# Performance work log

Hardware: AMD Instinct MI355X
Metric: run time of the kernel (lower is better)

Reference implementation:

```python
import jax, jax.numpy as jnp
import numpy as np

H = 512   # n_hidden
V = 32000 # n_words
T1 = 128  # encoder length
T2 = 64   # decoder length
B = 32    # batch


def _gru_cell(x, h, W_ih, W_hh, b_ih, b_hh):
    # PyTorch GRUCell math. x: [B, in], h: [B, H]
    gi = x @ W_ih.T + b_ih            # [B, 3H]
    gh = h @ W_hh.T + b_hh            # [B, 3H]
    i_r, i_z, i_n = jnp.split(gi, 3, axis=-1)
    h_r, h_z, h_n = jnp.split(gh, 3, axis=-1)
    r = jax.nn.sigmoid(i_r + h_r)
    z = jax.nn.sigmoid(i_z + h_z)
    n = jnp.tanh(i_n + r * h_n)
    return (1.0 - z) * n + z * h


def setup_inputs() -> dict:
    key = jax.random.key(0)
    ks = jax.random.split(key, 18)
    s = 0.05
    f32 = jnp.float32
    return {
        "decoder_inputs": jax.random.randint(ks[0], (T2, B), 0, V),
        "state": jax.random.normal(ks[1], (2, B, H), f32),
        "encoder_outputs": jax.random.normal(ks[2], (T1, B, H), f32),
        "emb": jax.random.normal(ks[3], (V, H), f32) * s,
        "wa_W": jax.random.normal(ks[4], (H, 2 * H), f32) * s,
        "wa_b": jax.random.normal(ks[5], (H,), f32) * s,
        "va_W": jax.random.normal(ks[6], (1, H), f32) * s,
        "W_ih0": jax.random.normal(ks[7], (3 * H, 2 * H), f32) * s,
        "W_hh0": jax.random.normal(ks[8], (3 * H, H), f32) * s,
        "b_ih0": jax.random.normal(ks[9], (3 * H,), f32) * s,
        "b_hh0": jax.random.normal(ks[10], (3 * H,), f32) * s,
        "W_ih1": jax.random.normal(ks[11], (3 * H, H), f32) * s,
        "W_hh1": jax.random.normal(ks[12], (3 * H, H), f32) * s,
        "b_ih1": jax.random.normal(ks[13], (3 * H,), f32) * s,
        "b_hh1": jax.random.normal(ks[14], (3 * H,), f32) * s,
        "out_W": jax.random.normal(ks[15], (V, H), f32) * s,
        "out_b": jax.random.normal(ks[16], (V,), f32) * s,
    }


def reference(decoder_inputs, state, encoder_outputs, emb, wa_W, wa_b, va_W,
              W_ih0, W_hh0, b_ih0, b_hh0, W_ih1, W_hh1, b_ih1, b_hh1,
              out_W, out_b):
    x = emb[decoder_inputs]                               # [T2, B, H]
    # wa(concat([xt_rep, enc])) == xt @ Wx.T + enc @ We.T + b  (split the weight)
    Wx = wa_W[:, :H]                                      # [H, H]
    We = wa_W[:, H:]                                      # [H, H]
    enc_proj = jnp.einsum('tbh,oh->tbo', encoder_outputs, We) + wa_b  # [T1,B,H]
    va = va_W[0]                                          # [H]

    def step(h, xt):  # h: [2,B,H], xt: [B,H]
        u = jnp.tanh(xt @ Wx.T + enc_proj)                # [T1, B, H]
        e = jnp.einsum('tbh,h->tb', u, va)                # [T1, B]
        score = jax.nn.softmax(e, axis=0)                 # softmax over T1
        att_v = jnp.einsum('tbh,tb->bh', encoder_outputs, score)  # [B, H]
        gin = jnp.concatenate([xt, att_v], axis=-1)       # [B, 2H]
        h0 = _gru_cell(gin, h[0], W_ih0, W_hh0, b_ih0, b_hh0)
        h1 = _gru_cell(h0, h[1], W_ih1, W_hh1, b_ih1, b_hh1)
        return jnp.stack([h0, h1]), (h1, score)

    h_final, (ys, scores) = jax.lax.scan(step, state, x)  # ys: [T2, B, H]
    y = jnp.einsum('tbh,vh->tbv', ys, out_W) + out_b      # [T2, B, V]
    last_score = scores[-1][:, :, None]                   # [T1, B, 1] (torch returns last-step score)
    return y, h_final, last_score
```

## Files before the change

### kernel.cpp

```cpp
#include <hip/hip_runtime.h>
#include <hip/hip_bf16.h>
#include <stdint.h>

#define HH   512
#define VV   32000
#define T1N  128
#define T2N  64
#define BB   32

typedef __attribute__((ext_vector_type(8))) short short8;
typedef __attribute__((ext_vector_type(4))) float f32x4;

__device__ __forceinline__ ushort f2b(float f) {
  unsigned u = __float_as_uint(f);
  unsigned r = (u + 0x7fffu + ((u >> 16) & 1u)) >> 16;
  return (ushort)r;
}
__device__ __forceinline__ float blo(unsigned u){ return __uint_as_float(u << 16); }
__device__ __forceinline__ float bhi(unsigned u){ return __uint_as_float(u & 0xffff0000u); }

__device__ __forceinline__ float fast_tanh(float x) {
  float ax = fabsf(x);
  float e  = __expf(-2.f * ax);
  float t  = (1.f - e) / (1.f + e);
  return x < 0.f ? -t : t;
}
__device__ __forceinline__ float fsig(float x) { return 1.f / (1.f + __expf(-x)); }

__global__ __launch_bounds__(256) void k_cvt(const float* __restrict__ s, ushort* __restrict__ d, int n) {
  int i = (blockIdx.x * 256 + threadIdx.x) * 4;
  if (i < n) {
    float4 v = *(const float4*)(s + i);
    ushort4 o = { f2b(v.x), f2b(v.y), f2b(v.z), f2b(v.w) };
    *(ushort4*)(d + i) = o;
  }
}

__global__ __launch_bounds__(256) void k_cvt_wa(const float* __restrict__ wa,
                                                ushort* __restrict__ Wx, ushort* __restrict__ We) {
  int i = (blockIdx.x * 256 + threadIdx.x) * 4;
  int half = (i >= HH * HH);
  int j = i & (HH * HH - 1);
  int o = j >> 9, c = j & 511;
  const float* s = wa + (size_t)o * 1024 + c + (half ? 512 : 0);
  float4 v = *(const float4*)s;
  ushort4 ov = { f2b(v.x), f2b(v.y), f2b(v.z), f2b(v.w) };
  *(ushort4*)((half ? We : Wx) + j) = ov;
}

__global__ __launch_bounds__(256) void k_embed(const int* __restrict__ toks, const float* __restrict__ emb,
                                               ushort* __restrict__ ginB) {
  int i = (blockIdx.x * 256 + threadIdx.x) * 4;
  int row = i >> 9, c = i & 511;
  int tok = toks[row];
  float4 v = *(const float4*)(emb + (size_t)tok * HH + c);
  ushort4 ov = { f2b(v.x), f2b(v.y), f2b(v.z), f2b(v.w) };
  *(ushort4*)(ginB + (size_t)row * 1024 + c) = ov;
}

__global__ __launch_bounds__(256) void k_gemm(const ushort* __restrict__ A, int lda,
                                              const ushort* __restrict__ B,
                                              const float* __restrict__ bias,
                                              float* __restrict__ C, int ldc, int K) {
  __shared__ ushort sA[128 * 32];
  __shared__ ushort sB[128 * 32];
  const int tid  = threadIdx.x;
  const int bm   = blockIdx.y * 128;
  const int bn   = blockIdx.x * 128;
  const int lane = tid & 63;
  const int wave = tid >> 6;
  const int wm   = (wave >> 1) * 64;
  const int wn   = (wave & 1) * 64;
  const int m16  = lane & 15;
  const int quad = lane >> 4;

  f32x4 acc[4][4] = {};

  for (int k0 = 0; k0 < K; k0 += 32) {
#pragma unroll
    for (int q = 0; q < 2; ++q) {
      int idx = q * 256 + tid;
      int row = idx >> 2;
      int kc  = (idx & 3) << 3;
      uint4 va = *(const uint4*)(A + (size_t)(bm + row) * lda + k0 + kc);
      *(uint4*)(&sA[idx * 8]) = va;
      uint4 vb = *(const uint4*)(B + (size_t)(bn + row) * K + k0 + kc);
      *(uint4*)(&sB[idx * 8]) = vb;
    }
    __syncthreads();
    short8 a[4], b[4];
#pragma unroll
    for (int i = 0; i < 4; ++i)
      a[i] = *(const short8*)(&sA[(wm + i * 16 + m16) * 32 + quad * 8]);
#pragma unroll
    for (int j = 0; j < 4; ++j)
      b[j] = *(const short8*)(&sB[(wn + j * 16 + m16) * 32 + quad * 8]);
#pragma unroll
    for (int i = 0; i < 4; ++i)
#pragma unroll
      for (int j = 0; j < 4; ++j)
        acc[i][j] = __builtin_amdgcn_mfma_f32_16x16x32_bf16(a[i], b[j], acc[i][j], 0, 0, 0);
    __syncthreads();
  }
#pragma unroll
  for (int i = 0; i < 4; ++i) {
    int gm = bm + wm + i * 16 + quad * 4;
#pragma unroll
    for (int j = 0; j < 4; ++j) {
      int gn = bn + wn + j * 16 + m16;
      float bv = bias ? bias[gn] : 0.f;
#pragma unroll
      for (int r = 0; r < 4; ++r)
        C[(size_t)(gm + r) * ldc + gn] = acc[i][j][r] + bv;
    }
  }
}

__global__ __launch_bounds__(256) void k_gemm_b16(const ushort* __restrict__ A, int lda,
                                                  const ushort* __restrict__ B,
                                                  const float* __restrict__ bias,
                                                  ushort* __restrict__ C, int ldc, int K) {
  __shared__ ushort sA[128 * 32];
  __shared__ ushort sB[128 * 32];
  const int tid  = threadIdx.x;
  const int bm   = blockIdx.y * 128;
  const int bn   = blockIdx.x * 128;
  const int lane = tid & 63;
  const int wave = tid >> 6;
  const int wm   = (wave >> 1) * 64;
  const int wn   = (wave & 1) * 64;
  const int m16  = lane & 15;
  const int quad = lane >> 4;

  f32x4 acc[4][4] = {};

  for (int k0 = 0; k0 < K; k0 += 32) {
#pragma unroll
    for (int q = 0; q < 2; ++q) {
      int idx = q * 256 + tid;
      int row = idx >> 2;
      int kc  = (idx & 3) << 3;
      uint4 va = *(const uint4*)(A + (size_t)(bm + row) * lda + k0 + kc);
      *(uint4*)(&sA[idx * 8]) = va;
      uint4 vb = *(const uint4*)(B + (size_t)(bn + row) * K + k0 + kc);
      *(uint4*)(&sB[idx * 8]) = vb;
    }
    __syncthreads();
    short8 a[4], b[4];
#pragma unroll
    for (int i = 0; i < 4; ++i)
      a[i] = *(const short8*)(&sA[(wm + i * 16 + m16) * 32 + quad * 8]);
#pragma unroll
    for (int j = 0; j < 4; ++j)
      b[j] = *(const short8*)(&sB[(wn + j * 16 + m16) * 32 + quad * 8]);
#pragma unroll
    for (int i = 0; i < 4; ++i)
#pragma unroll
      for (int j = 0; j < 4; ++j)
        acc[i][j] = __builtin_amdgcn_mfma_f32_16x16x32_bf16(a[i], b[j], acc[i][j], 0, 0, 0);
    __syncthreads();
  }
#pragma unroll
  for (int i = 0; i < 4; ++i) {
    int gm = bm + wm + i * 16 + quad * 4;
#pragma unroll
    for (int j = 0; j < 4; ++j) {
      int gn = bn + wn + j * 16 + m16;
      float bv = bias ? bias[gn] : 0.f;
#pragma unroll
      for (int r = 0; r < 4; ++r)
        C[(size_t)(gm + r) * ldc + gn] = f2b(acc[i][j][r] + bv);
    }
  }
}

__global__ __launch_bounds__(256) void k_scores(const float* __restrict__ xproj,
                                                const float* __restrict__ encp,
                                                const float* __restrict__ vaW,
                                                float* __restrict__ e) {
  int t2g = blockIdx.x >> 5;
  int b   = blockIdx.x & 31;
  __shared__ float sx[4][512];
  int tid = threadIdx.x;
  for (int i = tid; i < 4 * 512; i += 256) {
    int tt = i >> 9, h = i & 511;
    sx[tt][h] = xproj[((size_t)(t2g * 4 + tt) * BB + b) * HH + h];
  }
  __syncthreads();
  int lane = tid & 63, w = tid >> 6;
  int h8 = lane * 8;
  float va[8];
#pragma unroll
  for (int j = 0; j < 8; ++j) va[j] = vaW[h8 + j];
  for (int t1 = w; t1 < T1N; t1 += 4) {
    const float* ep = encp + ((size_t)t1 * BB + b) * HH + h8;
    float ev[8];
    *(float4*)&ev[0] = *(const float4*)ep;
    *(float4*)&ev[4] = *(const float4*)(ep + 4);
    float s0 = 0, s1 = 0, s2 = 0, s3 = 0;
#pragma unroll
    for (int j = 0; j < 8; ++j) {
      float epj = ev[j], vj = va[j];
      s0 += fast_tanh(sx[0][h8 + j] + epj) * vj;
      s1 += fast_tanh(sx[1][h8 + j] + epj) * vj;
      s2 += fast_tanh(sx[2][h8 + j] + epj) * vj;
      s3 += fast_tanh(sx[3][h8 + j] + epj) * vj;
    }
#pragma unroll
    for (int off = 32; off; off >>= 1) {
      s0 += __shfl_down(s0, off);
      s1 += __shfl_down(s1, off);
      s2 += __shfl_down(s2, off);
      s3 += __shfl_down(s3, off);
    }
    if (lane == 0) {
      size_t base = ((size_t)(t2g * 4) * BB + b) * T1N + t1;
      e[base]                 = s0;
      e[base + 1 * BB * T1N]  = s1;
      e[base + 2 * BB * T1N]  = s2;
      e[base + 3 * BB * T1N]  = s3;
    }
  }
}

__global__ __launch_bounds__(128) void k_softmax(const float* __restrict__ e, float* __restrict__ score,
                                                 float* __restrict__ out_last) {
  int row = blockIdx.x;
  int tid = threadIdx.x;
  float v = e[(size_t)row * T1N + tid];
  __shared__ float red[128];
  red[tid] = v; __syncthreads();
  for (int s = 64; s; s >>= 1) { if (tid < s) red[tid] = fmaxf(red[tid], red[tid + s]); __syncthreads(); }
  float mx = red[0]; __syncthreads();
  float p = __expf(v - mx);
  red[tid] = p; __syncthreads();
  for (int s = 64; s; s >>= 1) { if (tid < s) red[tid] += red[tid + s]; __syncthreads(); }
  float sc = p / red[0];
  score[(size_t)row * T1N + tid] = sc;
  if ((row >> 5) == T2N - 1) out_last[tid * BB + (row & 31)] = sc;
}

__global__ __launch_bounds__(256) void k_attv(const float* __restrict__ enc, const float* __restrict__ score,
                                              ushort* __restrict__ ginB) {
  int t2g = blockIdx.x >> 5;
  int b   = blockIdx.x & 31;
  __shared__ float ssc[8][T1N];
  int tid = threadIdx.x;
  for (int i = tid; i < 8 * T1N; i += 256) {
    int j = i >> 7, t1 = i & 127;
    ssc[j][t1] = score[((size_t)(t2g * 8 + j) * BB + b) * T1N + t1];
  }
  __syncthreads();
  float a0[8] = {}, a1[8] = {};
  for (int t1 = 0; t1 < T1N; ++t1) {
    const float* er = enc + ((size_t)t1 * BB + b) * HH;
    float e0 = er[tid], e1 = er[tid + 256];
#pragma unroll
    for (int j = 0; j < 8; ++j) { a0[j] += e0 * ssc[j][t1]; a1[j] += e1 * ssc[j][t1]; }
  }
#pragma unroll
  for (int j = 0; j < 8; ++j) {
    size_t r = (size_t)(t2g * 8 + j) * BB + b;
    ginB[r * 1024 + 512 + tid]       = f2b(a0[j]);
    ginB[r * 1024 + 512 + tid + 256] = f2b(a1[j]);
  }
}

__device__ __forceinline__ void gru_pair(uint gr, uint gz, uint gn, uint hr, uint hz, uint hn,
                                         float hold0, float hold1, float& o0, float& o1) {
  float r0 = fsig(blo(gr) + blo(hr));
  float r1 = fsig(bhi(gr) + bhi(hr));
  float z0 = fsig(blo(gz) + blo(hz));
  float z1 = fsig(bhi(gz) + bhi(hz));
  float n0 = fast_tanh(blo(gn) + r0 * blo(hn));
  float n1 = fast_tanh(bhi(gn) + r1 * bhi(hn));
  o0 = (1.f - z0) * n0 + z0 * hold0;
  o1 = (1.f - z1) * n1 + z1 * hold1;
}

__global__ __launch_bounds__(256) void k_stepA(
    int t,
    const ushort* __restrict__ Whh0B, const ushort* __restrict__ Whh1B,
    const float* __restrict__ bhh0, const float* __restrict__ bhh1,
    const ushort* __restrict__ gi1x, const ushort* __restrict__ gh1x_in,
    const float* __restrict__ h1_in,
    const float* __restrict__ state1,
    const ushort* __restrict__ h0B_in,
    ushort* __restrict__ gh0x_out, ushort* __restrict__ gh1x_out,
    float* __restrict__ h1_out, ushort* __restrict__ ys_out) {
  __shared__ ushort sH1[32 * 520];
  const int tid = threadIdx.x;
  const int blk = blockIdx.x;

  if (t == 0) {
    for (int i = tid; i < 16384; i += 256) {
      int b = i >> 9, k = i & 511;
      sH1[b * 520 + k] = f2b(state1[i]);
    }
  } else {
    const int k0 = tid * 2;
#pragma unroll 4
    for (int b = 0; b < 32; ++b) {
      const ushort* gi = gi1x + b * 1536 + k0;
      const ushort* gh = gh1x_in + b * 1536 + k0;
      uint gir = *(const uint*)(gi);
      uint giz = *(const uint*)(gi + 512);
      uint gin = *(const uint*)(gi + 1024);
      uint hr  = *(const uint*)(gh);
      uint hz  = *(const uint*)(gh + 512);
      uint hn  = *(const uint*)(gh + 1024);
      float2 hold = *(const float2*)(h1_in + b * 512 + k0);
      float o0, o1;
      gru_pair(gir, giz, gin, hr, hz, hn, hold.x, hold.y, o0, o1);
      uint hb = (uint)f2b(o0) | ((uint)f2b(o1) << 16);
      *(uint*)(&sH1[b * 520 + k0]) = hb;
      if (blk == b) {
        *(float2*)(h1_out + b * 512 + k0) = make_float2(o0, o1);
        *(uint*)(ys_out + b * 512 + k0) = hb;
      }
    }
  }
  __syncthreads();

  const int lane = tid & 63, wave = tid >> 6;
  const int bt = wave & 1, nt = wave >> 1;
  const int m16 = lane & 15, quad = lane >> 4;
  const int nrow = blk * 32 + nt * 16 + m16;

  f32x4 acc0 = {0.f, 0.f, 0.f, 0.f}, acc1 = {0.f, 0.f, 0.f, 0.f};
  const ushort* Arow0 = h0B_in + (bt * 16 + m16) * 512 + quad * 8;
  const ushort* Brow0 = Whh0B + (size_t)nrow * 512 + quad * 8;
  const ushort* Brow1 = Whh1B + (size_t)nrow * 512 + quad * 8;
  const ushort* sArow1 = &sH1[(bt * 16 + m16) * 520 + quad * 8];
#pragma unroll 4
  for (int kc = 0; kc < 16; ++kc) {
    short8 a0 = *(const short8*)(Arow0 + kc * 32);
    short8 b0 = *(const short8*)(Brow0 + kc * 32);
    acc0 = __builtin_amdgcn_mfma_f32_16x16x32_bf16(a0, b0, acc0, 0, 0, 0);
    short8 a1 = *(const short8*)(sArow1 + kc * 32);
    short8 b1 = *(const short8*)(Brow1 + kc * 32);
    acc1 = __builtin_amdgcn_mfma_f32_16x16x32_bf16(a1, b1, acc1, 0, 0, 0);
  }
  float bv0 = bhh0[nrow], bv1 = bhh1[nrow];
  int brow = bt * 16 + quad * 4;
#pragma unroll
  for (int r = 0; r < 4; ++r) {
    gh0x_out[(brow + r) * 1536 + nrow] = f2b(acc0[r] + bv0);
    gh1x_out[(brow + r) * 1536 + nrow] = f2b(acc1[r] + bv1);
  }
}

__global__ __launch_bounds__(256) void k_stepB(
    int t,
    const ushort* __restrict__ Wih1B, const float* __restrict__ bih1,
    const ushort* __restrict__ gi0B, const ushort* __restrict__ gh0x,
    const float* __restrict__ h0_in,
    float* __restrict__ h0_out, ushort* __restrict__ h0B_out,
    ushort* __restrict__ gi1x_out) {
  __shared__ ushort sH0[32 * 520];
  const int tid = threadIdx.x;
  const int blk = blockIdx.x;
  const ushort* gi0t = gi0B + (size_t)t * 32 * 1536;

  const int k0 = tid * 2;
#pragma unroll 4
  for (int b = 0; b < 32; ++b) {
    const ushort* gi = gi0t + b * 1536 + k0;
    const ushort* gh = gh0x + b * 1536 + k0;
    uint gir = *(const uint*)(gi);
    uint giz = *(const uint*)(gi + 512);
    uint gin = *(const uint*)(gi + 1024);
    uint hr  = *(const uint*)(gh);
    uint hz  = *(const uint*)(gh + 512);
    uint hn  = *(const uint*)(gh + 1024);
    float2 hold = *(const float2*)(h0_in + b * 512 + k0);
    float o0, o1;
    gru_pair(gir, giz, gin, hr, hz, hn, hold.x, hold.y, o0, o1);
    uint hb = (uint)f2b(o0) | ((uint)f2b(o1) << 16);
    *(uint*)(&sH0[b * 520 + k0]) = hb;
    if (blk == b) {
      *(float2*)(h0_out + b * 512 + k0) = make_float2(o0, o1);
      *(uint*)(h0B_out + b * 512 + k0) = hb;
    }
  }
  __syncthreads();

  const int lane = tid & 63, wave = tid >> 6;
  const int bt = wave & 1, nt = wave >> 1;
  const int m16 = lane & 15, quad = lane >> 4;
  const int nrow = blk * 32 + nt * 16 + m16;

  f32x4 acc = {0.f, 0.f, 0.f, 0.f};
  const ushort* Brow = Wih1B + (size_t)nrow * 512 + quad * 8;
  const ushort* sArow = &sH0[(bt * 16 + m16) * 520 + quad * 8];
#pragma unroll 4
  for (int kc = 0; kc < 16; ++kc) {
    short8 a = *(const short8*)(sArow + kc * 32);
    short8 b = *(const short8*)(Brow + kc * 32);
    acc = __builtin_amdgcn_mfma_f32_16x16x32_bf16(a, b, acc, 0, 0, 0);
  }
  float bv = bih1[nrow];
  int brow = bt * 16 + quad * 4;
#pragma unroll
  for (int r = 0; r < 4; ++r)
    gi1x_out[(brow + r) * 1536 + nrow] = f2b(acc[r] + bv);
}

__global__ __launch_bounds__(256) void k_final(
    const ushort* __restrict__ gi1x, const ushort* __restrict__ gh1x,
    const float* __restrict__ h1_in, const float* __restrict__ h0_fin,
    float* __restrict__ out_h, ushort* __restrict__ ys_out) {
  const int b = blockIdx.x;
  const int k0 = threadIdx.x * 2;
  const ushort* gi = gi1x + b * 1536 + k0;
  const ushort* gh = gh1x + b * 1536 + k0;
  uint gir = *(const uint*)(gi);
  uint giz = *(const uint*)(gi + 512);
  uint gin = *(const uint*)(gi + 1024);
  uint hr  = *(const uint*)(gh);
  uint hz  = *(const uint*)(gh + 512);
  uint hn  = *(const uint*)(gh + 1024);
  float2 hold = *(const float2*)(h1_in + b * 512 + k0);
  float o0, o1;
  gru_pair(gir, giz, gin, hr, hz, hn, hold.x, hold.y, o0, o1);
  *(uint*)(ys_out + b * 512 + k0) = (uint)f2b(o0) | ((uint)f2b(o1) << 16);
  out_h[16384 + b * 512 + k0]     = o0;
  out_h[16384 + b * 512 + k0 + 1] = o1;
  float2 h0p = *(const float2*)(h0_fin + b * 512 + k0);
  *(float2*)(out_h + b * 512 + k0) = h0p;
}

extern "C" void kernel_launch(void* const* d_in, const int* in_sizes, int n_in,
                              void* d_out, int out_size, void* d_ws, size_t ws_size,
                              hipStream_t stream) {
  const int*   toks  = (const int*)d_in[0];
  const float* state = (const float*)d_in[1];
  const float* enc   = (const float*)d_in[2];
  const float* emb   = (const float*)d_in[3];
  const float* wa_W  = (const float*)d_in[4];
  const float* wa_b  = (const float*)d_in[5];
  const float* va    = (const float*)d_in[6];
  const float* b_ih0 = (const float*)d_in[9];
  const float* b_hh0 = (const float*)d_in[10];
  const float* b_ih1 = (const float*)d_in[13];
  const float* b_hh1 = (const float*)d_in[14];
  const float* out_W = (const float*)d_in[15];
  const float* out_b = (const float*)d_in[16];
  const float* W_ih0 = (const float*)d_in[7];
  const float* W_hh0 = (const float*)d_in[8];
  const float* W_ih1 = (const float*)d_in[11];
  const float* W_hh1 = (const float*)d_in[12];

  float* y_out  = (float*)d_out;
  float* h_out  = y_out + (size_t)T2N * BB * VV;
  float* ls_out = h_out + 2 * BB * HH;

  char* ws = (char*)d_ws;
  size_t off = 0;
  auto alloc = [&](size_t bytes) -> void* {
    void* p = ws + off;
    off += (bytes + 255) & ~(size_t)255;
    return p;
  };
  ushort* encB   = (ushort*)alloc((size_t)T1N * BB * HH * 2);
  ushort* ginB   = (ushort*)alloc((size_t)T2N * BB * 2 * HH * 2);
  ushort* WeB    = (ushort*)alloc((size_t)HH * HH * 2);
  ushort* WxB    = (ushort*)alloc((size_t)HH * HH * 2);
  ushort* Wih0B  = (ushort*)alloc((size_t)3 * HH * 2 * HH * 2);
  ushort* Whh0B  = (ushort*)alloc((size_t)3 * HH * HH * 2);
  ushort* Wih1B  = (ushort*)alloc((size_t)3 * HH * HH * 2);
  ushort* Whh1B  = (ushort*)alloc((size_t)3 * HH * HH * 2);
  ushort* outWB  = (ushort*)alloc((size_t)VV * HH * 2);
  ushort* stateB = (ushort*)alloc((size_t)BB * HH * 2);
  float* encproj = (float*)alloc((size_t)T1N * BB * HH * 4);
  float* xproj   = (float*)alloc((size_t)T2N * BB * HH * 4);
  float* eM      = (float*)alloc((size_t)T2N * BB * T1N * 4);
  float* score   = (float*)alloc((size_t)T2N * BB * T1N * 4);
  ushort* gi0B   = (ushort*)alloc((size_t)T2N * BB * 3 * HH * 2);
  ushort* gh0x   = (ushort*)alloc((size_t)BB * 3 * HH * 2);
  ushort* gh1buf0 = (ushort*)alloc((size_t)BB * 3 * HH * 2);
  ushort* gh1buf1 = (ushort*)alloc((size_t)BB * 3 * HH * 2);
  ushort* gi1x   = (ushort*)alloc((size_t)BB * 3 * HH * 2);
  float* h0buf0  = (float*)alloc((size_t)BB * HH * 4);
  float* h0buf1  = (float*)alloc((size_t)BB * HH * 4);
  float* h1buf0  = (float*)alloc((size_t)BB * HH * 4);
  float* h1buf1  = (float*)alloc((size_t)BB * HH * 4);
  ushort* h0bufB0 = (ushort*)alloc((size_t)BB * HH * 2);
  ushort* h0bufB1 = (ushort*)alloc((size_t)BB * HH * 2);
  ushort* ysB    = (ushort*)alloc((size_t)T2N * BB * HH * 2);

  ushort* gh1buf[2]  = {gh1buf0, gh1buf1};
  float*  h0buf[2]   = {h0buf0, h0buf1};
  float*  h1buf[2]   = {h1buf0, h1buf1};
  ushort* h0bufB[2]  = {h0bufB0, h0bufB1};

  k_cvt<<<VV * HH / 1024, 256, 0, stream>>>(out_W, outWB, VV * HH);
  k_cvt<<<T1N * BB * HH / 1024, 256, 0, stream>>>(enc, encB, T1N * BB * HH);
  k_cvt<<<3 * HH * 2 * HH / 1024, 256, 0, stream>>>(W_ih0, Wih0B, 3 * HH * 2 * HH);
  k_cvt<<<3 * HH * HH / 1024, 256, 0, stream>>>(W_hh0, Whh0B, 3 * HH * HH);
  k_cvt<<<3 * HH * HH / 1024, 256, 0, stream>>>(W_ih1, Wih1B, 3 * HH * HH);
  k_cvt<<<3 * HH * HH / 1024, 256, 0, stream>>>(W_hh1, Whh1B, 3 * HH * HH);
  k_cvt<<<BB * HH / 1024, 256, 0, stream>>>(state, stateB, BB * HH);
  k_cvt_wa<<<2 * HH * HH / 1024, 256, 0, stream>>>(wa_W, WxB, WeB);
  k_embed<<<T2N * BB * HH / 1024, 256, 0, stream>>>(toks, emb, ginB);

  k_gemm<<<dim3(HH / 128, T1N * BB / 128), 256, 0, stream>>>(encB, HH, WeB, wa_b, encproj, HH, HH);
  k_gemm<<<dim3(HH / 128, T2N * BB / 128), 256, 0, stream>>>(ginB, 2 * HH, WxB, nullptr, xproj, HH, HH);

  k_scores<<<512, 256, 0, stream>>>(xproj, encproj, va, eM);
  k_softmax<<<T2N * BB, 128, 0, stream>>>(eM, score, ls_out);
  k_attv<<<256, 256, 0, stream>>>(enc, score, ginB);

  k_gemm_b16<<<dim3(3 * HH / 128, T2N * BB / 128), 256, 0, stream>>>(ginB, 2 * HH, Wih0B, b_ih0, gi0B, 3 * HH, 2 * HH);

  for (int t = 0; t < T2N; ++t) {
    const float*  h1_in  = (t <= 1) ? (state + BB * HH) : h1buf[t & 1];
    const ushort* h0B_in = (t == 0) ? stateB : h0bufB[(t + 1) & 1];
    ushort* ys_prev = (t == 0) ? ysB : (ysB + (size_t)(t - 1) * BB * HH);
    k_stepA<<<48, 256, 0, stream>>>(t, Whh0B, Whh1B, b_hh0, b_hh1,
                                    gi1x, gh1buf[(t + 1) & 1],
                                    h1_in, state + BB * HH, h0B_in,
                                    gh0x, gh1buf[t & 1],
                                    h1buf[(t + 1) & 1], ys_prev);
    const float* h0_in = (t == 0) ? state : h0buf[(t + 1) & 1];
    k_stepB<<<48, 256, 0, stream>>>(t, Wih1B, b_ih1, gi0B, gh0x, h0_in,
                                    h0buf[t & 1], h0bufB[t & 1], gi1x);
  }
  k_final<<<32, 256, 0, stream>>>(gi1x, gh1buf[1], h1buf[0], h0buf[1],
                                  h_out, ysB + (size_t)63 * BB * HH);

  k_gemm<<<dim3(VV / 128, T2N * BB / 128), 256, 0, stream>>>(ysB, HH, outWB, out_b, y_out, VV, HH);
}
```

Before: 3.877 ms.

## Fuse per-timestep GRU kernels into one persistent cooperative kernel with grid sync

Replaces the 128 per-step kernel launches (stepA/stepB per timestep) plus the final kernel with a single cooperative persistent kernel of 48 blocks. Inside it, grid.sync() separates the two phases of each timestep, and the final layer-1 GRU update runs at the end. This removes launch overhead and the inter-kernel gaps on the serial recurrence. The cost is a software grid barrier, whose latency may approach the launch gap, and it relies on all 48 blocks being co-resident.

Result: slower. 4.500 ms (+16.1%).

```diff
diff --git a/kernel.cpp b/kernel.cpp
--- a/kernel.cpp
+++ b/kernel.cpp
@@ -1,6 +1,9 @@
 #include <hip/hip_runtime.h>
 #include <hip/hip_bf16.h>
+#include <hip/hip_cooperative_groups.h>
 #include <stdint.h>
+
+namespace cg = cooperative_groups;
 
 #define HH   512
 #define VV   32000
@@ -278,156 +281,162 @@
   o1 = (1.f - z1) * n1 + z1 * hold1;
 }
 
-__global__ __launch_bounds__(256) void k_stepA(
-    int t,
-    const ushort* __restrict__ Whh0B, const ushort* __restrict__ Whh1B,
-    const float* __restrict__ bhh0, const float* __restrict__ bhh1,
-    const ushort* __restrict__ gi1x, const ushort* __restrict__ gh1x_in,
-    const float* __restrict__ h1_in,
-    const float* __restrict__ state1,
-    const ushort* __restrict__ h0B_in,
-    ushort* __restrict__ gh0x_out, ushort* __restrict__ gh1x_out,
-    float* __restrict__ h1_out, ushort* __restrict__ ys_out) {
-  __shared__ ushort sH1[32 * 520];
-  const int tid = threadIdx.x;
-  const int blk = blockIdx.x;
-
-  if (t == 0) {
-    for (int i = tid; i < 16384; i += 256) {
-      int b = i >> 9, k = i & 511;
-      sH1[b * 520 + k] = f2b(state1[i]);
-    }
-  } else {
-    const int k0 = tid * 2;
-#pragma unroll 4
-    for (int b = 0; b < 32; ++b) {
-      const ushort* gi = gi1x + b * 1536 + k0;
-      const ushort* gh = gh1x_in + b * 1536 + k0;
-      uint gir = *(const uint*)(gi);
-      uint giz = *(const uint*)(gi + 512);
-      uint gin = *(const uint*)(gi + 1024);
-      uint hr  = *(const uint*)(gh);
-      uint hz  = *(const uint*)(gh + 512);
-      uint hn  = *(const uint*)(gh + 1024);
-      float2 hold = *(const float2*)(h1_in + b * 512 + k0);
-      float o0, o1;
-      gru_pair(gir, giz, gin, hr, hz, hn, hold.x, hold.y, o0, o1);
-      uint hb = (uint)f2b(o0) | ((uint)f2b(o1) << 16);
-      *(uint*)(&sH1[b * 520 + k0]) = hb;
-      if (blk == b) {
-        *(float2*)(h1_out + b * 512 + k0) = make_float2(o0, o1);
-        *(uint*)(ys_out + b * 512 + k0) = hb;
-      }
-    }
-  }
-  __syncthreads();
-
+struct RecurP {
+  const ushort* Whh0B; const ushort* Whh1B; const ushort* Wih1B;
+  const float* bhh0; const float* bhh1; const float* bih1;
+  const ushort* gi0B;
+  const float* state;
+  const ushort* stateB;
+  ushort* gh0x;
+  ushort* gh1b0; ushort* gh1b1;
+  ushort* gi1x;
+  float* h0b0; float* h0b1;
+  float* h1b0; float* h1b1;
+  ushort* h0B0; ushort* h0B1;
+  float* h_out;
+  ushort* ysB;
+};
+
+__global__ __launch_bounds__(256, 1) void k_recur(RecurP p) {
+  cg::grid_group grid = cg::this_grid();
+  __shared__ ushort sH[32 * 520];
+  const int tid  = threadIdx.x;
+  const int blk  = blockIdx.x;
   const int lane = tid & 63, wave = tid >> 6;
   const int bt = wave & 1, nt = wave >> 1;
   const int m16 = lane & 15, quad = lane >> 4;
   const int nrow = blk * 32 + nt * 16 + m16;
-
-  f32x4 acc0 = {0.f, 0.f, 0.f, 0.f}, acc1 = {0.f, 0.f, 0.f, 0.f};
-  const ushort* Arow0 = h0B_in + (bt * 16 + m16) * 512 + quad * 8;
-  const ushort* Brow0 = Whh0B + (size_t)nrow * 512 + quad * 8;
-  const ushort* Brow1 = Whh1B + (size_t)nrow * 512 + quad * 8;
-  const ushort* sArow1 = &sH1[(bt * 16 + m16) * 520 + quad * 8];
+  const int k0 = tid * 2;
+  const float* state1 = p.state + BB * HH;
+
+  const float bv0 = p.bhh0[nrow];
+  const float bv1 = p.bhh1[nrow];
+  const float bvi = p.bih1[nrow];
+  const int brow = bt * 16 + quad * 4;
+
+#pragma unroll 1
+  for (int t = 0; t < T2N; ++t) {
+    const int par = t & 1;
+    if (t == 0) {
+      for (int i = tid; i < 16384; i += 256) {
+        int b = i >> 9, k = i & 511;
+        sH[b * 520 + k] = f2b(state1[i]);
+      }
+    } else {
+      const ushort* gh1in = par ? p.gh1b0 : p.gh1b1;
+      const float*  h1in  = (t <= 1) ? state1 : (par ? p.h1b1 : p.h1b0);
+      float*        h1out = par ? p.h1b0 : p.h1b1;
+      ushort*       ysprev = p.ysB + (size_t)(t - 1) * BB * HH;
 #pragma unroll 4
-  for (int kc = 0; kc < 16; ++kc) {
-    short8 a0 = *(const short8*)(Arow0 + kc * 32);
-    short8 b0 = *(const short8*)(Brow0 + kc * 32);
-    acc0 = __builtin_amdgcn_mfma_f32_16x16x32_bf16(a0, b0, acc0, 0, 0, 0);
-    short8 a1 = *(const short8*)(sArow1 + kc * 32);
-    short8 b1 = *(const short8*)(Brow1 + kc * 32);
-    acc1 = __builtin_amdgcn_mfma_f32_16x16x32_bf16(a1, b1, acc1, 0, 0, 0);
-  }
-  float bv0 = bhh0[nrow], bv1 = bhh1[nrow];
-  int brow = bt * 16 + quad * 4;
-#pragma unroll
-  for (int r = 0; r < 4; ++r) {
-    gh0x_out[(brow + r) * 1536 + nrow] = f2b(acc0[r] + bv0);
-    gh1x_out[(brow + r) * 1536 + nrow] = f2b(acc1[r] + bv1);
-  }
-}
-
-__global__ __launch_bounds__(256) void k_stepB(
-    int t,
-    const ushort* __restrict__ Wih1B, const float* __restrict__ bih1,
-    const ushort* __restrict__ gi0B, const ushort* __restrict__ gh0x,
-    const float* __restrict__ h0_in,
-    float* __restrict__ h0_out, ushort* __restrict__ h0B_out,
-    ushort* __restrict__ gi1x_out) {
-  __shared__ ushort sH0[32 * 520];
-  const int tid = threadIdx.x;
-  const int blk = blockIdx.x;
-  const ushort* gi0t = gi0B + (size_t)t * 32 * 1536;
-
-  const int k0 = tid * 2;
+      for (int b = 0; b < 32; ++b) {
+        const ushort* gi = p.gi1x + b * 1536 + k0;
+        const ushort* gh = gh1in + b * 1536 + k0;
+        uint gir = *(const uint*)(gi);
+        uint giz = *(const uint*)(gi + 512);
+        uint gin = *(const uint*)(gi + 1024);
+        uint hr  = *(const uint*)(gh);
+        uint hz  = *(const uint*)(gh + 512);
+        uint hn  = *(const uint*)(gh + 1024);
+        float2 hold = *(const float2*)(h1in + b * 512 + k0);
+        float o0, o1;
+        gru_pair(gir, giz, gin, hr, hz, hn, hold.x, hold.y, o0, o1);
+        uint hb = (uint)f2b(o0) | ((uint)f2b(o1) << 16);
+        *(uint*)(&sH[b * 520 + k0]) = hb;
+        if (blk == b) {
+          *(float2*)(h1out + b * 512 + k0) = make_float2(o0, o1);
+          *(uint*)(ysprev + b * 512 + k0) = hb;
+        }
+      }
+    }
+    __syncthreads();
+
+    {
+      const ushort* h0Bin = (t == 0) ? p.stateB : (par ? p.h0B0 : p.h0B1);
+      ushort* gh1out = par ? p.gh1b1 : p.gh1b0;
+      f32x4 acc0 = {0.f, 0.f, 0.f, 0.f}, acc1 = {0.f, 0.f, 0.f, 0.f};
+      const ushort* Arow0  = h0Bin + (bt * 16 + m16) * 512 + quad * 8;
+      const ushort* Brow0  = p.Whh0B + (size_t)nrow * 512 + quad * 8;
+      const ushort* Brow1  = p.Whh1B + (size_t)nrow * 512 + quad * 8;
+      const ushort* sArow1 = &sH[(bt * 16 + m16) * 520 + quad * 8];
 #pragma unroll 4
-  for (int b = 0; b < 32; ++b) {
-    const ushort* gi = gi0t + b * 1536 + k0;
-    const ushort* gh = gh0x + b * 1536 + k0;
+      for (int kc = 0; kc < 16; ++kc) {
+        short8 a0 = *(const short8*)(Arow0 + kc * 32);
+        short8 b0 = *(const short8*)(Brow0 + kc * 32);
+        acc0 = __builtin_amdgcn_mfma_f32_16x16x32_bf16(a0, b0, acc0, 0, 0, 0);
+        short8 a1 = *(const short8*)(sArow1 + kc * 32);
+        short8 b1 = *(const short8*)(Brow1 + kc * 32);
+        acc1 = __builtin_amdgcn_mfma_f32_16x16x32_bf16(a1, b1, acc1, 0, 0, 0);
+      }
+#pragma unroll
+      for (int r = 0; r < 4; ++r) {
+        p.gh0x[(brow + r) * 1536 + nrow] = f2b(acc0[r] + bv0);
+        gh1out[(brow + r) * 1536 + nrow] = f2b(acc1[r] + bv1);
+      }
+    }
+    grid.sync();
+
+    {
+      const ushort* gi0t  = p.gi0B + (size_t)t * 32 * 1536;
+      const float*  h0in  = (t == 0) ? p.state : (par ? p.h0b0 : p.h0b1);
+      float*        h0out = par ? p.h0b1 : p.h0b0;
+      ushort*       h0Bout = par ? p.h0B1 : p.h0B0;
+#pragma unroll 4
+      for (int b = 0; b < 32; ++b) {
+        const ushort* gi = gi0t + b * 1536 + k0;
+        const ushort* gh = p.gh0x + b * 1536 + k0;
+        uint gir = *(const uint*)(gi);
+        uint giz = *(const uint*)(gi + 512);
+        uint gin = *(const uint*)(gi + 1024);
+        uint hr  = *(const uint*)(gh);
+        uint hz  = *(const uint*)(gh + 512);
+        uint hn  = *(const uint*)(gh + 1024);
+        float2 hold = *(const float2*)(h0in + b * 512 + k0);
+        float o0, o1;
+        gru_pair(gir, giz, gin, hr, hz, hn, hold.x, hold.y, o0, o1);
+        uint hb = (uint)f2b(o0) | ((uint)f2b(o1) << 16);
+        *(uint*)(&sH[b * 520 + k0]) = hb;
+        if (blk == b) {
+          *(float2*)(h0out + b * 512 + k0) = make_float2(o0, o1);
+          *(uint*)(h0Bout + b * 512 + k0) = hb;
+        }
+      }
+      __syncthreads();
+
+      f32x4 acc = {0.f, 0.f, 0.f, 0.f};
+      const ushort* Brow  = p.Wih1B + (size_t)nrow * 512 + quad * 8;
+      const ushort* sArow = &sH[(bt * 16 + m16) * 520 + quad * 8];
+#pragma unroll 4
+      for (int kc = 0; kc < 16; ++kc) {
+        short8 a = *(const short8*)(sArow + kc * 32);
+        short8 b = *(const short8*)(Brow + kc * 32);
+        acc = __builtin_amdgcn_mfma_f32_16x16x32_bf16(a, b, acc, 0, 0, 0);
+      }
+#pragma unroll
+      for (int r = 0; r < 4; ++r)
+        p.gi1x[(brow + r) * 1536 + nrow] = f2b(acc[r] + bvi);
+    }
+    grid.sync();
+  }
+
+  if (blk < 32) {
+    const int b = blk;
+    const ushort* gi = p.gi1x + b * 1536 + k0;
+    const ushort* gh = p.gh1b1 + b * 1536 + k0;
     uint gir = *(const uint*)(gi);
     uint giz = *(const uint*)(gi + 512);
     uint gin = *(const uint*)(gi + 1024);
     uint hr  = *(const uint*)(gh);
     uint hz  = *(const uint*)(gh + 512);
     uint hn  = *(const uint*)(gh + 1024);
-    float2 hold = *(const float2*)(h0_in + b * 512 + k0);
+    float2 hold = *(const float2*)(p.h1b0 + b * 512 + k0);
     float o0, o1;
     gru_pair(gir, giz, gin, hr, hz, hn, hold.x, hold.y, o0, o1);
-    uint hb = (uint)f2b(o0) | ((uint)f2b(o1) << 16);
-    *(uint*)(&sH0[b * 520 + k0]) = hb;
-    if (blk == b) {
-      *(float2*)(h0_out + b * 512 + k0) = make_float2(o0, o1);
-      *(uint*)(h0B_out + b * 512 + k0) = hb;
-    }
-  }
-  __syncthreads();
-
-  const int lane = tid & 63, wave = tid >> 6;
-  const int bt = wave & 1, nt = wave >> 1;
-  const int m16 = lane & 15, quad = lane >> 4;
-  const int nrow = blk * 32 + nt * 16 + m16;
-
-  f32x4 acc = {0.f, 0.f, 0.f, 0.f};
-  const ushort* Brow = Wih1B + (size_t)nrow * 512 + quad * 8;
-  const ushort* sArow = &sH0[(bt * 16 + m16) * 520 + quad * 8];
-#pragma unroll 4
-  for (int kc = 0; kc < 16; ++kc) {
-    short8 a = *(const short8*)(sArow + kc * 32);
-    short8 b = *(const short8*)(Brow + kc * 32);
-    acc = __builtin_amdgcn_mfma_f32_16x16x32_bf16(a, b, acc, 0, 0, 0);
-  }
-  float bv = bih1[nrow];
-  int brow = bt * 16 + quad * 4;
-#pragma unroll
-  for (int r = 0; r < 4; ++r)
-    gi1x_out[(brow + r) * 1536 + nrow] = f2b(acc[r] + bv);
-}
-
-__global__ __launch_bounds__(256) void k_final(
-    const ushort* __restrict__ gi1x, const ushort* __restrict__ gh1x,
-    const float* __restrict__ h1_in, const float* __restrict__ h0_fin,
-    float* __restrict__ out_h, ushort* __restrict__ ys_out) {
-  const int b = blockIdx.x;
-  const int k0 = threadIdx.x * 2;
-  const ushort* gi = gi1x + b * 1536 + k0;
-  const ushort* gh = gh1x + b * 1536 + k0;
-  uint gir = *(const uint*)(gi);
-  uint giz = *(const uint*)(gi + 512);
-  uint gin = *(const uint*)(gi + 1024);
-  uint hr  = *(const uint*)(gh);
-  uint hz  = *(const uint*)(gh + 512);
-  uint hn  = *(const uint*)(gh + 1024);
-  float2 hold = *(const float2*)(h1_in + b * 512 + k0);
-  float o0, o1;
-  gru_pair(gir, giz, gin, hr, hz, hn, hold.x, hold.y, o0, o1);
-  *(uint*)(ys_out + b * 512 + k0) = (uint)f2b(o0) | ((uint)f2b(o1) << 16);
-  out_h[16384 + b * 512 + k0]     = o0;
-  out_h[16384 + b * 512 + k0 + 1] = o1;
-  float2 h0p = *(const float2*)(h0_fin + b * 512 + k0);
-  *(float2*)(out_h + b * 512 + k0) = h0p;
+    *(uint*)(p.ysB + (size_t)63 * BB * HH + b * 512 + k0) = (uint)f2b(o0) | ((uint)f2b(o1) << 16);
+    p.h_out[16384 + b * 512 + k0]     = o0;
+    p.h_out[16384 + b * 512 + k0 + 1] = o1;
+    float2 h0p = *(const float2*)(p.h0b1 + b * 512 + k0);
+    *(float2*)(p.h_out + b * 512 + k0) = h0p;
+  }
 }
 
 extern "C" void kernel_launch(void* const* d_in, const int* in_sizes, int n_in,
@@ -489,11 +498,6 @@
   ushort* h0bufB1 = (ushort*)alloc((size_t)BB * HH * 2);
   ushort* ysB    = (ushort*)alloc((size_t)T2N * BB * HH * 2);
 
-  ushort* gh1buf[2]  = {gh1buf0, gh1buf1};
-  float*  h0buf[2]   = {h0buf0, h0buf1};
-  float*  h1buf[2]   = {h1buf0, h1buf1};
-  ushort* h0bufB[2]  = {h0bufB0, h0bufB1};
-
   k_cvt<<<VV * HH / 1024, 256, 0, stream>>>(out_W, outWB, VV * HH);
   k_cvt<<<T1N * BB * HH / 1024, 256, 0, stream>>>(enc, encB, T1N * BB * HH);
   k_cvt<<<3 * HH * 2 * HH / 1024, 256, 0, stream>>>(W_ih0, Wih0B, 3 * HH * 2 * HH);
@@ -513,21 +517,20 @@
 
   k_gemm_b16<<<dim3(3 * HH / 128, T2N * BB / 128), 256, 0, stream>>>(ginB, 2 * HH, Wih0B, b_ih0, gi0B, 3 * HH, 2 * HH);
 
-  for (int t = 0; t < T2N; ++t) {
-    const float*  h1_in  = (t <= 1) ? (state + BB * HH) : h1buf[t & 1];
-    const ushort* h0B_in = (t == 0) ? stateB : h0bufB[(t + 1) & 1];
-    ushort* ys_prev = (t == 0) ? ysB : (ysB + (size_t)(t - 1) * BB * HH);
-    k_stepA<<<48, 256, 0, stream>>>(t, Whh0B, Whh1B, b_hh0, b_hh1,
-                                    gi1x, gh1buf[(t + 1) & 1],
-                                    h1_in, state + BB * HH, h0B_in,
-                                    gh0x, gh1buf[t & 1],
-                                    h1buf[(t + 1) & 1], ys_prev);
-    const float* h0_in = (t == 0) ? state : h0buf[(t + 1) & 1];
-    k_stepB<<<48, 256, 0, stream>>>(t, Wih1B, b_ih1, gi0B, gh0x, h0_in,
-                                    h0buf[t & 1], h0bufB[t & 1], gi1x);
-  }
-  k_final<<<32, 256, 0, stream>>>(gi1x, gh1buf[1], h1buf[0], h0buf[1],
-                                  h_out, ysB + (size_t)63 * BB * HH);
+  RecurP rp;
+  rp.Whh0B = Whh0B; rp.Whh1B = Whh1B; rp.Wih1B = Wih1B;
+  rp.bhh0 = b_hh0; rp.bhh1 = b_hh1; rp.bih1 = b_ih1;
+  rp.gi0B = gi0B;
+  rp.state = state; rp.stateB = stateB;
+  rp.gh0x = gh0x;
+  rp.gh1b0 = gh1buf0; rp.gh1b1 = gh1buf1;
+  rp.gi1x = gi1x;
+  rp.h0b0 = h0buf0; rp.h0b1 = h0buf1;
+  rp.h1b0 = h1buf0; rp.h1b1 = h1buf1;
+  rp.h0B0 = h0bufB0; rp.h0B1 = h0bufB1;
+  rp.h_out = h_out; rp.ysB = ysB;
+  void* kargs[] = { &rp };
+  hipLaunchCooperativeKernel((const void*)k_recur, dim3(48), dim3(256), kargs, 0, stream);
 
   k_gemm<<<dim3(VV / 128, T2N * BB / 128), 256, 0, stream>>>(ysB, HH, outWB, out_b, y_out, VV, HH);
 }
```
